# Optimization experiments

Measured on AMD Instinct MI355X. Metric: run time of the kernel, lower is better.

Reference implementation:

```python
import jax, jax.numpy as jnp
import numpy as np

RANK = 32
BASE_RES = 4


def interp_matrix(n_out, r):
    # align_corners=True bilinear sampling of an r-point axis at cell-centered
    # coords (i+0.5)/n_out mapped to [-1,1]; t = (i+0.5)/n_out * (r-1).
    t = (jnp.arange(n_out, dtype=jnp.float32) + 0.5) / n_out * (r - 1)
    i0 = jnp.clip(jnp.floor(t), 0, r - 2).astype(jnp.int32)
    frac = t - i0.astype(jnp.float32)
    w = (jax.nn.one_hot(i0, r, dtype=jnp.float32) * (1.0 - frac)[:, None]
         + jax.nn.one_hot(i0 + 1, r, dtype=jnp.float32) * frac[:, None])
    return w  # (n_out, r)


def setup_inputs() -> dict:
    key = jax.random.key(0)
    ks = jax.random.split(key, 6)
    B, Cin, Cout, H, W = 8, 128, 128, 128, 128
    fan_in = Cin * BASE_RES * BASE_RES
    stdv = 1.0 / np.sqrt(Cin)
    v = jax.random.normal(ks[0], (B, Cin, H, W), dtype=jnp.float32)
    k1 = jax.random.normal(ks[1], (RANK, Cin, BASE_RES, BASE_RES), dtype=jnp.float32) / np.sqrt(fan_in)
    k2 = jax.random.normal(ks[2], (RANK, Cout, BASE_RES, BASE_RES), dtype=jnp.float32) / np.sqrt(fan_in)
    conv_w = jax.random.uniform(ks[3], (Cout, Cin), dtype=jnp.float32, minval=-stdv, maxval=stdv)
    conv_b = jax.random.uniform(ks[4], (Cout,), dtype=jnp.float32, minval=-stdv, maxval=stdv)
    bias = jax.random.uniform(ks[5], (Cout, 1, 1), dtype=jnp.float32, minval=-stdv, maxval=stdv)
    return {"v": v, "k1": k1, "k2": k2, "conv_w": conv_w, "conv_b": conv_b, "bias": bias}


def reference(v, k1, k2, conv_w, conv_b, bias):
    B, Cin, H, W = v.shape
    r = k1.shape[-1]
    wy = interp_matrix(H, r)  # (H, r)
    wx = interp_matrix(W, r)  # (W, r)
    # grid_sample(kernel, cell-centered grid, align_corners=True, bilinear)
    k1i = jnp.einsum('hp,wq,ripq->rihw', wy, wx, k1)  # (R, Cin, H, W)
    k2i = jnp.einsum('hp,wq,ropq->rohw', wy, wx, k2)  # (R, Cout, H, W)
    vr = jnp.einsum('rihw,bihw->br', k1i, v) / (H * W)  # (B, R)
    out = jnp.einsum('rohw,br->bohw', k2i, vr)          # (B, Cout, H, W)
    out = out + jnp.einsum('oi,bihw->bohw', conv_w, v) + conv_b[None, :, None, None]
    out = out + bias[None]
    return out
```

## Files before the change

kernel.cpp:

```cpp
#include <hip/hip_runtime.h>


typedef __attribute__((ext_vector_type(8))) short bf16x8;
typedef __attribute__((ext_vector_type(4))) float f32x4;
typedef unsigned int u32;
typedef unsigned short u16;

static __device__ __forceinline__ u16 f2bf(float x) {
    union { float f; u32 u; } a; a.f = x;
    u32 r = a.u + 0x7fffu + ((a.u >> 16) & 1u);
    return (u16)(r >> 16);
}
static __device__ __forceinline__ float bf2f(u16 h) {
    union { u32 u; float f; } a; a.u = ((u32)h) << 16;
    return a.f;
}

__global__ __launch_bounds__(256) void kA_reduceS(const float* __restrict__ v,
                                                  float* __restrict__ S)
{
    int bid = blockIdx.x;
    const float* img = v + ((size_t)bid << 14);
    int tid  = threadIdx.x;
    int wave = tid >> 6, lane = tid & 63;

    int w0 = lane * 2;
    float wxA[4], wxB[4];
    {
        float t0 = (w0 + 0.5f) * (3.0f / 128.0f);
        int j0 = (int)t0; j0 = j0 > 2 ? 2 : j0;
        float f0 = t0 - (float)j0;
        float t1 = (w0 + 1.5f) * (3.0f / 128.0f);
        int j1 = (int)t1; j1 = j1 > 2 ? 2 : j1;
        float f1 = t1 - (float)j1;
#pragma unroll
        for (int q = 0; q < 4; ++q) {
            wxA[q] = (q == j0) ? (1.0f - f0) : ((q == j0 + 1) ? f0 : 0.0f);
            wxB[q] = (q == j1) ? (1.0f - f1) : ((q == j1 + 1) ? f1 : 0.0f);
        }
    }

    float acc[4][4] = {};
#pragma unroll 4
    for (int h = wave; h < 128; h += 4) {
        float2 px = *(const float2*)(img + h * 128 + w0);
        float part[4];
#pragma unroll
        for (int q = 0; q < 4; ++q) part[q] = px.x * wxA[q] + px.y * wxB[q];
        float t = (h + 0.5f) * (3.0f / 128.0f);
        int i0 = (int)t; i0 = i0 > 2 ? 2 : i0;
        float fr = t - (float)i0;
#pragma unroll
        for (int p = 0; p < 4; ++p) {
            float wyp = (p == i0) ? (1.0f - fr) : ((p == i0 + 1) ? fr : 0.0f);
#pragma unroll
            for (int q = 0; q < 4; ++q) acc[p][q] += wyp * part[q];
        }
    }

#pragma unroll
    for (int p = 0; p < 4; ++p)
#pragma unroll
        for (int q = 0; q < 4; ++q) {
            float s = acc[p][q];
#pragma unroll
            for (int m = 32; m >= 1; m >>= 1) s += __shfl_xor(s, m, 64);
            acc[p][q] = s;
        }

    __shared__ float red[4][16];
    if (lane == 0) {
#pragma unroll
        for (int p = 0; p < 4; ++p)
#pragma unroll
            for (int q = 0; q < 4; ++q) red[wave][p * 4 + q] = acc[p][q];
    }
    __syncthreads();
    if (tid < 16) {
        float s = red[0][tid] + red[1][tid] + red[2][tid] + red[3][tid];
        S[(bid << 4) + tid] = s;
    }
}

__global__ __launch_bounds__(256) void kB_small(const float* __restrict__ S,
                                                const float* __restrict__ k1,
                                                const float* __restrict__ k2,
                                                const float* __restrict__ conv_w,
                                                const float* __restrict__ conv_b,
                                                const float* __restrict__ bias,
                                                float* __restrict__ T,
                                                u16* __restrict__ Wh,
                                                u16* __restrict__ Wl)
{
    int b = blockIdx.x;
    int tid = threadIdx.x;
    __shared__ float Ss[2048];
    __shared__ float vrs[32];

    const float* Sb = S + b * 2048;
#pragma unroll
    for (int it = 0; it < 2; ++it) {
        int f = (it * 256 + tid) * 4;
        *(float4*)&Ss[f] = *(const float4*)&Sb[f];
    }
    __syncthreads();

    {
        int r = tid >> 3, j = tid & 7;
        const float* k1r = k1 + r * 2048 + j * 256;
        const float* Sj  = Ss + j * 256;
        float partial = 0.0f;
#pragma unroll 4
        for (int e = 0; e < 256; e += 4) {
            float4 a  = *(const float4*)&k1r[e];
            float4 s4 = *(const float4*)&Sj[e];
            partial += a.x * s4.x + a.y * s4.y + a.z * s4.z + a.w * s4.w;
        }
        partial += __shfl_xor(partial, 1, 64);
        partial += __shfl_xor(partial, 2, 64);
        partial += __shfl_xor(partial, 4, 64);
        if (j == 0) vrs[r] = partial * (1.0f / 16384.0f);
    }
    __syncthreads();

    {
        int f0 = tid * 8;
        int o  = tid >> 1;
        float cb = conv_b[o] + bias[o];
        float acc[8] = {};
        for (int rr = 0; rr < 32; ++rr) {
            float vv = vrs[rr];
            const float* k2r = k2 + rr * 2048 + f0;
            float4 a0 = *(const float4*)&k2r[0];
            float4 a1 = *(const float4*)&k2r[4];
            acc[0] += vv * a0.x; acc[1] += vv * a0.y;
            acc[2] += vv * a0.z; acc[3] += vv * a0.w;
            acc[4] += vv * a1.x; acc[5] += vv * a1.y;
            acc[6] += vv * a1.z; acc[7] += vv * a1.w;
        }
        float* Tb = T + b * 2048 + f0;
        float4 r0, r1;
        r0.x = acc[0] + cb; r0.y = acc[1] + cb; r0.z = acc[2] + cb; r0.w = acc[3] + cb;
        r1.x = acc[4] + cb; r1.y = acc[5] + cb; r1.z = acc[6] + cb; r1.w = acc[7] + cb;
        *(float4*)&Tb[0] = r0;
        *(float4*)&Tb[4] = r1;
    }

    {
        int ks = tid >> 6, l = tid & 63;
        int o = (b << 4) + (l & 15);
        int ibase = ks * 32 + ((l >> 4) << 3);
        const float* src = conv_w + o * 128 + ibase;
        float4 c0 = *(const float4*)src;
        float4 c1 = *(const float4*)(src + 4);
        float xs[8] = {c0.x, c0.y, c0.z, c0.w, c1.x, c1.y, c1.z, c1.w};
        union { u16 s[8]; bf16x8 v; } ph, pl;
#pragma unroll
        for (int j = 0; j < 8; ++j) {
            u16 hi = f2bf(xs[j]);
            ph.s[j] = hi;
            pl.s[j] = f2bf(xs[j] - bf2f(hi));
        }
        int didx = (((b * 4 + ks) * 64) + l) * 8;
        *(bf16x8*)(Wh + didx) = ph.v;
        *(bf16x8*)(Wl + didx) = pl.v;
    }
}

__global__ __launch_bounds__(256, 4) void kC_mfma(const float* __restrict__ v,
                                                  const u16* __restrict__ Wh,
                                                  const u16* __restrict__ Wl,
                                                  const float* __restrict__ T,
                                                  float* __restrict__ out)
{
    __shared__ u16 vt[16384];
    __shared__ float U[128][4];

    int h = blockIdx.x, b = blockIdx.y;
    int tid = threadIdx.x;
    int lane = tid & 63, wid = tid >> 6;

    const float* vb = v + ((size_t)b << 21) + h * 128;

    {
        int w = tid & 127, ib = tid >> 7;
        unsigned sw = (unsigned)(w & 15);
        unsigned rowbase = (unsigned)w * 256 + (unsigned)ib * 8;
#pragma unroll
        for (int it = 0; it < 16; ++it) {
            int i0 = it * 8 + ib * 4;
            float x0 = vb[(size_t)(i0 + 0) * 16384 + w];
            float x1 = vb[(size_t)(i0 + 1) * 16384 + w];
            float x2 = vb[(size_t)(i0 + 2) * 16384 + w];
            float x3 = vb[(size_t)(i0 + 3) * 16384 + w];
            u32 p0 = (u32)f2bf(x0) | ((u32)f2bf(x1) << 16);
            u32 p1 = (u32)f2bf(x2) | ((u32)f2bf(x3) << 16);
            unsigned byteoff = rowbase + ((((unsigned)it) ^ sw) << 4);
            *(uint2*)((char*)vt + byteoff) = make_uint2(p0, p1);
        }
    }

    {
        float t = (h + 0.5f) * (3.0f / 128.0f);
        int i0 = (int)t; i0 = i0 > 2 ? 2 : i0;
        float fr = t - (float)i0;
        if (tid < 128) {
            const float* Tb = T + b * 2048 + tid * 16;
            float4 r0 = *(const float4*)&Tb[0];
            float4 r1 = *(const float4*)&Tb[4];
            float4 r2 = *(const float4*)&Tb[8];
            float4 r3 = *(const float4*)&Tb[12];
            float wy0 = (i0 == 0) ? (1.0f - fr) : 0.0f;
            float wy1 = (i0 == 1) ? (1.0f - fr) : ((i0 == 0) ? fr : 0.0f);
            float wy2 = (i0 == 2) ? (1.0f - fr) : ((i0 == 1) ? fr : 0.0f);
            float wy3 = (i0 == 2) ? fr : 0.0f;
            U[tid][0] = wy0 * r0.x + wy1 * r1.x + wy2 * r2.x + wy3 * r3.x;
            U[tid][1] = wy0 * r0.y + wy1 * r1.y + wy2 * r2.y + wy3 * r3.y;
            U[tid][2] = wy0 * r0.z + wy1 * r1.z + wy2 * r2.z + wy3 * r3.z;
            U[tid][3] = wy0 * r0.w + wy1 * r1.w + wy2 * r2.w + wy3 * r3.w;
        }
    }
    __syncthreads();

    int mh = wid >> 1, nh = wid & 1;
    int g = lane >> 4, ln = lane & 15;

    f32x4 acc[4][4];
#pragma unroll
    for (int mt = 0; mt < 4; ++mt)
#pragma unroll
        for (int nt = 0; nt < 4; ++nt)
            acc[mt][nt] = (f32x4){0.f, 0.f, 0.f, 0.f};

#pragma unroll
    for (int ks = 0; ks < 4; ++ks) {
        bf16x8 Ah[4], Al[4];
#pragma unroll
        for (int mt = 0; mt < 4; ++mt) {
            int idx = ((((mh * 4 + mt) * 4 + ks) * 64) + lane) * 8;
            Ah[mt] = *(const bf16x8*)(Wh + idx);
            Al[mt] = *(const bf16x8*)(Wl + idx);
        }
#pragma unroll
        for (int nt = 0; nt < 4; ++nt) {
            unsigned wrow = (unsigned)(nh * 64 + nt * 16 + ln);
            unsigned byteoff = wrow * 256 + ((((unsigned)(ks * 4 + g)) ^ (unsigned)ln) << 4);
            bf16x8 Bf = *(const bf16x8*)((const char*)vt + byteoff);
#pragma unroll
            for (int mt = 0; mt < 4; ++mt) {
                acc[mt][nt] = __builtin_amdgcn_mfma_f32_16x16x32_bf16(Ah[mt], Bf, acc[mt][nt], 0, 0, 0);
                acc[mt][nt] = __builtin_amdgcn_mfma_f32_16x16x32_bf16(Al[mt], Bf, acc[mt][nt], 0, 0, 0);
            }
        }
    }

    float wqa[4][4];
#pragma unroll
    for (int nt = 0; nt < 4; ++nt) {
        int wn = nh * 64 + nt * 16 + ln;
        float tw = (wn + 0.5f) * (3.0f / 128.0f);
        int j0 = (int)tw; j0 = j0 > 2 ? 2 : j0;
        float fw = tw - (float)j0;
        wqa[nt][0] = (j0 == 0) ? (1.0f - fw) : 0.0f;
        wqa[nt][1] = (j0 == 1) ? (1.0f - fw) : ((j0 == 0) ? fw : 0.0f);
        wqa[nt][2] = (j0 == 2) ? (1.0f - fw) : ((j0 == 1) ? fw : 0.0f);
        wqa[nt][3] = (j0 == 2) ? fw : 0.0f;
    }

    float* ob = out + ((size_t)b << 21) + h * 128;
#pragma unroll
    for (int mt = 0; mt < 4; ++mt) {
#pragma unroll
        for (int r = 0; r < 4; ++r) {
            int o = mh * 64 + mt * 16 + g * 4 + r;
            float4 Uo = *(const float4*)&U[o][0];
            float* orow = ob + (size_t)o * 16384;
#pragma unroll
            for (int nt = 0; nt < 4; ++nt) {
                int wn = nh * 64 + nt * 16 + ln;
                float res = acc[mt][nt][r] + wqa[nt][0] * Uo.x + wqa[nt][1] * Uo.y
                                           + wqa[nt][2] * Uo.z + wqa[nt][3] * Uo.w;
                orow[wn] = res;
            }
        }
    }
}

extern "C" void kernel_launch(void* const* d_in, const int* in_sizes, int n_in,
                              void* d_out, int out_size, void* d_ws, size_t ws_size,
                              hipStream_t stream) {
    const float* v      = (const float*)d_in[0];
    const float* k1     = (const float*)d_in[1];
    const float* k2     = (const float*)d_in[2];
    const float* conv_w = (const float*)d_in[3];
    const float* conv_b = (const float*)d_in[4];
    const float* bias   = (const float*)d_in[5];
    float* out = (float*)d_out;

    float* S  = (float*)d_ws;
    float* T  = S + 16384;
    u16*   Wh = (u16*)((char*)d_ws + 131072);
    u16*   Wl = (u16*)((char*)d_ws + 163840);

    kA_reduceS<<<1024, 256, 0, stream>>>(v, S);
    kB_small<<<8, 256, 0, stream>>>(S, k1, k2, conv_w, conv_b, bias, T, Wh, Wl);
    kC_mfma<<<dim3(128, 8), 256, 0, stream>>>(v, Wh, Wl, T, out);
}
```

Before: 155.8 us.

## Split v transpose/bf16 conversion into separate kernel writing swizzled global buffer

Moves the fp32-to-bf16 transpose of v out of the MFMA kernel into a new kernel that writes the swizzled tile layout to a workspace buffer. The MFMA kernel then reads B fragments straight from global memory instead of LDS, dropping its large shared array. This is meant to raise occupancy and simplify the MFMA kernel. The cost is an extra launch plus a write and re-read of a 32 MB bf16 copy of v.

```diff
diff --git a/kernel.cpp b/kernel.cpp
--- a/kernel.cpp
+++ b/kernel.cpp
@@ -80,6 +80,41 @@
         float s = red[0][tid] + red[1][tid] + red[2][tid] + red[3][tid];
         S[(bid << 4) + tid] = s;
     }
+}
+
+__global__ __launch_bounds__(256) void kT_transpose(const float* __restrict__ v,
+                                                    u16* __restrict__ VT)
+{
+    __shared__ u16 vt[16384];
+
+    int h = blockIdx.x, b = blockIdx.y;
+    int tid = threadIdx.x;
+    const float* vb = v + ((size_t)b << 21) + h * 128;
+
+    {
+        int w = tid & 127, ib = tid >> 7;
+        unsigned sw = (unsigned)(w & 15);
+        unsigned rowbase = (unsigned)w * 256 + (unsigned)ib * 8;
+#pragma unroll
+        for (int it = 0; it < 16; ++it) {
+            int i0 = it * 8 + ib * 4;
+            float x0 = vb[(size_t)(i0 + 0) * 16384 + w];
+            float x1 = vb[(size_t)(i0 + 1) * 16384 + w];
+            float x2 = vb[(size_t)(i0 + 2) * 16384 + w];
+            float x3 = vb[(size_t)(i0 + 3) * 16384 + w];
+            u32 p0 = (u32)f2bf(x0) | ((u32)f2bf(x1) << 16);
+            u32 p1 = (u32)f2bf(x2) | ((u32)f2bf(x3) << 16);
+            unsigned byteoff = rowbase + ((((unsigned)it) ^ sw) << 4);
+            *(uint2*)((char*)vt + byteoff) = make_uint2(p0, p1);
+        }
+    }
+    __syncthreads();
+
+    uint4* dst = (uint4*)(VT + ((size_t)(b * 128 + h) << 14));
+    const uint4* src = (const uint4*)vt;
+#pragma unroll
+    for (int k = 0; k < 8; ++k)
+        dst[tid + 256 * k] = src[tid + 256 * k];
 }
 
 __global__ __launch_bounds__(256) void kB_small(const float* __restrict__ S,
@@ -167,38 +202,19 @@
     }
 }
 
-__global__ __launch_bounds__(256, 4) void kC_mfma(const float* __restrict__ v,
+__global__ __launch_bounds__(256, 4) void kC_mfma(const u16* __restrict__ VT,
                                                   const u16* __restrict__ Wh,
                                                   const u16* __restrict__ Wl,
                                                   const float* __restrict__ T,
                                                   float* __restrict__ out)
 {
-    __shared__ u16 vt[16384];
     __shared__ float U[128][4];
 
     int h = blockIdx.x, b = blockIdx.y;
     int tid = threadIdx.x;
     int lane = tid & 63, wid = tid >> 6;
 
-    const float* vb = v + ((size_t)b << 21) + h * 128;
-
-    {
-        int w = tid & 127, ib = tid >> 7;
-        unsigned sw = (unsigned)(w & 15);
-        unsigned rowbase = (unsigned)w * 256 + (unsigned)ib * 8;
-#pragma unroll
-        for (int it = 0; it < 16; ++it) {
-            int i0 = it * 8 + ib * 4;
-            float x0 = vb[(size_t)(i0 + 0) * 16384 + w];
-            float x1 = vb[(size_t)(i0 + 1) * 16384 + w];
-            float x2 = vb[(size_t)(i0 + 2) * 16384 + w];
-            float x3 = vb[(size_t)(i0 + 3) * 16384 + w];
-            u32 p0 = (u32)f2bf(x0) | ((u32)f2bf(x1) << 16);
-            u32 p1 = (u32)f2bf(x2) | ((u32)f2bf(x3) << 16);
-            unsigned byteoff = rowbase + ((((unsigned)it) ^ sw) << 4);
-            *(uint2*)((char*)vt + byteoff) = make_uint2(p0, p1);
-        }
-    }
+    const char* vtg = (const char*)(VT + ((size_t)(b * 128 + h) << 14));
 
     {
         float t = (h + 0.5f) * (3.0f / 128.0f);
@@ -220,7 +236,6 @@
             U[tid][3] = wy0 * r0.w + wy1 * r1.w + wy2 * r2.w + wy3 * r3.w;
         }
     }
-    __syncthreads();
 
     int mh = wid >> 1, nh = wid & 1;
     int g = lane >> 4, ln = lane & 15;
@@ -234,7 +249,7 @@
 
 #pragma unroll
     for (int ks = 0; ks < 4; ++ks) {
-        bf16x8 Ah[4], Al[4];
+        bf16x8 Ah[4], Al[4], Bf[4];
 #pragma unroll
         for (int mt = 0; mt < 4; ++mt) {
             int idx = ((((mh * 4 + mt) * 4 + ks) * 64) + lane) * 8;
@@ -245,14 +260,18 @@
         for (int nt = 0; nt < 4; ++nt) {
             unsigned wrow = (unsigned)(nh * 64 + nt * 16 + ln);
             unsigned byteoff = wrow * 256 + ((((unsigned)(ks * 4 + g)) ^ (unsigned)ln) << 4);
-            bf16x8 Bf = *(const bf16x8*)((const char*)vt + byteoff);
+            Bf[nt] = *(const bf16x8*)(vtg + byteoff);
+        }
+#pragma unroll
+        for (int nt = 0; nt < 4; ++nt)
 #pragma unroll
             for (int mt = 0; mt < 4; ++mt) {
-                acc[mt][nt] = __builtin_amdgcn_mfma_f32_16x16x32_bf16(Ah[mt], Bf, acc[mt][nt], 0, 0, 0);
-                acc[mt][nt] = __builtin_amdgcn_mfma_f32_16x16x32_bf16(Al[mt], Bf, acc[mt][nt], 0, 0, 0);
+                acc[mt][nt] = __builtin_amdgcn_mfma_f32_16x16x32_bf16(Ah[mt], Bf[nt], acc[mt][nt], 0, 0, 0);
+                acc[mt][nt] = __builtin_amdgcn_mfma_f32_16x16x32_bf16(Al[mt], Bf[nt], acc[mt][nt], 0, 0, 0);
             }
-        }
-    }
+    }
+
+    __syncthreads();
 
     float wqa[4][4];
 #pragma unroll
@@ -278,9 +297,8 @@
 #pragma unroll
             for (int nt = 0; nt < 4; ++nt) {
                 int wn = nh * 64 + nt * 16 + ln;
-                float res = acc[mt][nt][r] + wqa[nt][0] * Uo.x + wqa[nt][1] * Uo.y
-                                           + wqa[nt][2] * Uo.z + wqa[nt][3] * Uo.w;
-                orow[wn] = res;
+                orow[wn] = acc[mt][nt][r] + wqa[nt][0] * Uo.x + wqa[nt][1] * Uo.y
+                                          + wqa[nt][2] * Uo.z + wqa[nt][3] * Uo.w;
             }
         }
     }
@@ -298,11 +316,13 @@
     float* out = (float*)d_out;
 
     float* S  = (float*)d_ws;
-    float* T  = S + 16384;
+    float* T  = (float*)((char*)d_ws + 65536);
     u16*   Wh = (u16*)((char*)d_ws + 131072);
     u16*   Wl = (u16*)((char*)d_ws + 163840);
+    u16*   VT = (u16*)((char*)d_ws + 196608);
 
     kA_reduceS<<<1024, 256, 0, stream>>>(v, S);
+    kT_transpose<<<dim3(128, 8), 256, 0, stream>>>(v, VT);
     kB_small<<<8, 256, 0, stream>>>(S, k1, k2, conv_w, conv_b, bias, T, Wh, Wl);
-    kC_mfma<<<dim3(128, 8), 256, 0, stream>>>(v, Wh, Wl, T, out);
-}
+    kC_mfma<<<dim3(128, 8), 256, 0, stream>>>(VT, Wh, Wl, T, out);
+}
```

Result: slower. 166.8 us (+7.0%).
